# Optimization experiments

Measured on AMD Instinct MI355X. Metric: run time of the kernel, lower is better.

The kernel has to match this reference:

```python
import jax, jax.numpy as jnp
import numpy as np
from jax import lax


def setup_inputs() -> dict:
    key = jax.random.key(0)
    k1, k2 = jax.random.split(key)
    X = jax.random.normal(k1, (32, 64, 112, 112), dtype=jnp.float32)
    # module draws K ~ N(0, 0.01) each forward; we materialize it as a param
    K = 0.01 * jax.random.normal(k2, (128, 64, 3, 3), dtype=jnp.float32)
    return {"X": X, "K": K}


def reference(X, K):
    # Valid-padding cross-correlation, NCHW input, OIHW kernel, no bias.
    # Matches conv2d_multi_out: sum over in_channels, stack over out_channels.
    return lax.conv_general_dilated(
        X, K,
        window_strides=(1, 1),
        padding="VALID",
        dimension_numbers=("NCHW", "OIHW", "NCHW"),
    )
```

## Files before the change

### kernel.cpp

```cpp
#include <hip/hip_runtime.h>


typedef __attribute__((ext_vector_type(8)))  _Float16 f16x8;
typedef __attribute__((ext_vector_type(16))) float    f32x16;

typedef __attribute__((address_space(3))) uint       lds_u32;
typedef __attribute__((address_space(1))) const uint glb_u32;

constexpr int C_IN = 64, H = 112, W = 112;
constexpr int COUT = 128, OH = 110, OW = 110;
constexpr int NIMG = 32;
constexpr int KTOT = C_IN * 9;
constexpr int OSP  = OH * OW;
constexpr int SPTOT = NIMG * OSP;
constexpr int IMG_STRIDE = C_IN * H * W;
constexpr int CH_STRIDE  = H * W;
constexpr int XROW = W * C_IN;
constexpr int SLOTS = 136;
constexpr int UNITS = SLOTS * 8;
constexpr size_t A16_BYTES = (size_t)KTOT * COUT * 2;

__device__ __forceinline__ uint pkrtz_u32(float lo, float hi) {
    union { __fp16 __attribute__((ext_vector_type(2))) h; uint u; } c;
    c.h = __builtin_amdgcn_cvt_pkrtz(lo, hi);
    return c.u;
}

__global__ void prep_a(const float* __restrict__ Kw, _Float16* __restrict__ A16) {
    int idx = blockIdx.x * 256 + threadIdx.x;
    if (idx >= COUT * KTOT) return;
    int cout = idx / KTOT, k = idx - cout * KTOT;
    int c = k / 9, s = k - c * 9;
    int o = c >> 3, j = c & 7;
    A16[((size_t)(s * 8 + o) * COUT + cout) * 8 + j] = (_Float16)Kw[idx];
}

__global__ __launch_bounds__(256, 4)
void prep_x(const float* __restrict__ X, _Float16* __restrict__ X16t) {
    __shared__ _Float16 L[W * 72];
    const int t = threadIdx.x;
    const int n = blockIdx.x / H, h = blockIdx.x - n * H;
    const float* src = X + (size_t)n * IMG_STRIDE + (size_t)h * W;
    const int c = t >> 2, q = t & 3;
    const float* sc = src + (size_t)c * CH_STRIDE + q * 28;
#pragma unroll
    for (int v = 0; v < 7; v++) {
        float4 f = *reinterpret_cast<const float4*>(sc + v * 4);
        const int w0 = q * 28 + v * 4;
        L[(w0 + 0) * 72 + c] = (_Float16)f.x;
        L[(w0 + 1) * 72 + c] = (_Float16)f.y;
        L[(w0 + 2) * 72 + c] = (_Float16)f.z;
        L[(w0 + 3) * 72 + c] = (_Float16)f.w;
    }
    __syncthreads();
    _Float16* dst = X16t + ((size_t)n * H + h) * XROW;
#pragma unroll
    for (int r = 0; r < 4; r++) {
        const int u = r * 256 + t;
        if (u < 896) {
            const int w = u >> 3, sl = u & 7;
            *reinterpret_cast<f16x8*>(dst + (size_t)u * 8) =
                *reinterpret_cast<const f16x8*>(&L[w * 72 + sl * 8]);
        }
    }
}

__global__ __launch_bounds__(512, 4)
void conv_v13(const _Float16* __restrict__ X16t,
              const _Float16* __restrict__ A16,
              float* __restrict__ Out)
{
    __shared__ __align__(16) _Float16 Bs[2][SLOTS * 64];

    const int t = threadIdx.x;

    const int nwg = gridDim.x;
    const int q8 = nwg >> 3, r8 = nwg & 7;
    const int xcd = blockIdx.x & 7, idx8 = blockIdx.x >> 3;
    const int bid = (xcd < r8 ? xcd * (q8 + 1) : r8 * (q8 + 1) + (xcd - r8) * q8) + idx8;
    const int spBase = bid * 128;

    const int n0  = spBase / OSP;
    const int r0  = spBase - n0 * OSP;
    const int oh0 = r0 / OW;
    const int ow0 = r0 - oh0 * OW;
    const int seg1len = (109 - oh0) * 112 + (112 - ow0);

    const int lane = t & 63;
    const int wv   = t >> 6;
    const _Float16* sU0;
    const _Float16* sU1;
    const _Float16* sU2;
    {
        const int uu[3] = {t, t + 512, 1024 + (t & 63)};
        const _Float16* ss[3];
#pragma unroll
        for (int i = 0; i < 3; i++) {
            const int u  = uu[i];
            const int ws = u >> 3, oct = u & 7;
            const int so = (oct ^ (ws & 7)) * 8;
            size_t lin;
            if (ws < seg1len) {
                lin = (size_t)n0 * CH_STRIDE + (size_t)(oh0 * 112 + ow0 + ws);
            } else {
                const int nn = (n0 < NIMG - 1) ? n0 + 1 : n0;
                lin = (size_t)nn * CH_STRIDE + (size_t)(ws - seg1len);
            }
            ss[i] = X16t + lin * 64 + so;
        }
        sU0 = ss[0]; sU1 = ss[1]; sU2 = ss[2];
    }

    const int wq    = wv >> 1;
    const int wc    = wv & 1;
    const int frow  = lane & 31;
    const int khalf = lane >> 5;
    const size_t arow = (size_t)(wq * 32 + frow) * 8;

    int w0i, w1i;
    {
        const int ii[2] = {wc * 64 + frow, wc * 64 + 32 + frow};
        int wx[2];
#pragma unroll
        for (int i = 0; i < 2; i++) {
            const int spg = spBase + ii[i];
            const int n   = spg / OSP;
            const int r   = spg - n * OSP;
            const int oh  = r / OW;
            const int ow  = r - oh * OW;
            wx[i] = (n == n0) ? (oh - oh0) * 112 + (ow - ow0)
                              : seg1len + oh * 112 + ow;
        }
        w0i = wx[0]; w1i = wx[1];
    }

    f32x16 acc[2];
#pragma unroll
    for (int j = 0; j < 2; j++)
#pragma unroll
        for (int e = 0; e < 16; e++) acc[j][e] = 0.f;

    f16x8 aA[4], aB[4];

#define STAGE(R, B)                                                            \
    {                                                                          \
        __builtin_amdgcn_global_load_lds((const glb_u32*)(sU0 + (R) * XROW),   \
            (lds_u32*)(&Bs[B][(size_t)t * 8]), 16, 0, 0);                      \
        __builtin_amdgcn_global_load_lds((const glb_u32*)(sU1 + (R) * XROW),   \
            (lds_u32*)(&Bs[B][(size_t)(t + 512) * 8]), 16, 0, 0);              \
        if (wv == 0)                                                           \
            __builtin_amdgcn_global_load_lds((const glb_u32*)(sU2 + (R) * XROW), \
                (lds_u32*)(&Bs[B][(size_t)(1024 + lane) * 8]), 16, 0, 0);      \
    }

#define ALOAD(DST, S)                                                          \
    {                                                                          \
        _Pragma("unroll")                                                      \
        for (int kk = 0; kk < 4; kk++)                                         \
            DST[kk] = *reinterpret_cast<const f16x8*>(                         \
                &A16[(size_t)(((S) * 8 + kk * 2 + khalf) * COUT) * 8 + arow]); \
    }

#define MFMA_SH(KW, B, AREG)                                                   \
    {                                                                          \
        const int sa = w0i + (KW);                                             \
        const int sb = w1i + (KW);                                             \
        _Pragma("unroll")                                                      \
        for (int kk = 0; kk < 4; kk++) {                                       \
            const int oct = kk * 2 + khalf;                                    \
            f16x8 b0 = *reinterpret_cast<const f16x8*>(                        \
                &Bs[B][sa * 64 + ((oct ^ (sa & 7)) << 3)]);                    \
            f16x8 b1 = *reinterpret_cast<const f16x8*>(                        \
                &Bs[B][sb * 64 + ((oct ^ (sb & 7)) << 3)]);                    \
            acc[0] = __builtin_amdgcn_mfma_f32_32x32x16_f16(AREG[kk], b0, acc[0], 0, 0, 0); \
            acc[1] = __builtin_amdgcn_mfma_f32_32x32x16_f16(AREG[kk], b1, acc[1], 0, 0, 0); \
        }                                                                      \
    }

    ALOAD(aA, 0);
    STAGE(0, 0);
    __syncthreads();

    STAGE(1, 1);
    ALOAD(aB, 1); MFMA_SH(0, 0, aA);
    ALOAD(aA, 2); MFMA_SH(1, 0, aB);
    ALOAD(aB, 3); MFMA_SH(2, 0, aA);
    __syncthreads();

    STAGE(2, 0);
    ALOAD(aA, 4); MFMA_SH(0, 1, aB);
    ALOAD(aB, 5); MFMA_SH(1, 1, aA);
    ALOAD(aA, 6); MFMA_SH(2, 1, aB);
    __syncthreads();

    ALOAD(aB, 7); MFMA_SH(0, 0, aA);
    ALOAD(aA, 8); MFMA_SH(1, 0, aB);
    MFMA_SH(2, 0, aA);

#undef STAGE
#undef ALOAD
#undef MFMA_SH

#pragma unroll
    for (int j = 0; j < 2; j++) {
        const int sp2 = spBase + wc * 64 + j * 32 + frow;
        const int n2  = sp2 / OSP;
        const int r2  = sp2 - n2 * OSP;
        float* Ob = Out + (size_t)n2 * (COUT * (size_t)OSP) + r2;
        const int cbase = wq * 32 + 4 * khalf;
#pragma unroll
        for (int reg = 0; reg < 16; reg++) {
            const int crow = cbase + (reg & 3) + 8 * (reg >> 2);
            Ob[(size_t)crow * OSP] = acc[j][reg];
        }
    }
}

extern "C" void kernel_launch(void* const* d_in, const int* in_sizes, int n_in,
                              void* d_out, int out_size, void* d_ws, size_t ws_size,
                              hipStream_t stream) {
    const float* X  = (const float*)d_in[0];
    const float* Kw = (const float*)d_in[1];
    float* Out = (float*)d_out;
    _Float16* A16  = (_Float16*)d_ws;
    _Float16* X16t = (_Float16*)((char*)d_ws + A16_BYTES);

    prep_a<<<(COUT * KTOT + 255) / 256, 256, 0, stream>>>(Kw, A16);
    prep_x<<<NIMG * H, 256, 0, stream>>>(X, X16t);
    conv_v13<<<SPTOT / 128, 512, 0, stream>>>(X16t, A16, Out);
}
```

Before: 118.8 us.

## Double spatial tile to 256 per workgroup with 2x2 MFMA register tiling

Each workgroup now covers 256 output positions instead of 128. Each wave computes a 64-channel by 64-position block through a 2x2 set of 32x32 MFMA accumulators, where before it computed 32x64. This halves the number of workgroups, doubles the reuse of each A fragment and each B fragment per load, and cuts redundant halo staging. In exchange it costs more accumulator registers, doubles the LDS buffer size (which may lower occupancy), drops the A-register double buffering, and adds bounds checks for the partial last tile.

```diff
diff --git a/kernel.cpp b/kernel.cpp
--- a/kernel.cpp
+++ b/kernel.cpp
@@ -16,8 +16,9 @@
 constexpr int IMG_STRIDE = C_IN * H * W;
 constexpr int CH_STRIDE  = H * W;
 constexpr int XROW = W * C_IN;
-constexpr int SLOTS = 136;
-constexpr int UNITS = SLOTS * 8;
+constexpr int TILE = 256;
+constexpr int NWGM = (SPTOT + TILE - 1) / TILE;
+constexpr int SLOTS = 264;
 constexpr size_t A16_BYTES = (size_t)KTOT * COUT * 2;
 
 __device__ __forceinline__ uint pkrtz_u32(float lo, float hi) {
@@ -66,39 +67,35 @@
 }
 
 __global__ __launch_bounds__(512, 4)
-void conv_v13(const _Float16* __restrict__ X16t,
+void conv_v14(const _Float16* __restrict__ X16t,
               const _Float16* __restrict__ A16,
               float* __restrict__ Out)
 {
     __shared__ __align__(16) _Float16 Bs[2][SLOTS * 64];
 
     const int t = threadIdx.x;
+    const int lane = t & 63;
+    const int wv   = t >> 6;
 
     const int nwg = gridDim.x;
     const int q8 = nwg >> 3, r8 = nwg & 7;
     const int xcd = blockIdx.x & 7, idx8 = blockIdx.x >> 3;
     const int bid = (xcd < r8 ? xcd * (q8 + 1) : r8 * (q8 + 1) + (xcd - r8) * q8) + idx8;
-    const int spBase = bid * 128;
+    const int spBase = bid * TILE;
 
     const int n0  = spBase / OSP;
     const int r0  = spBase - n0 * OSP;
     const int oh0 = r0 / OW;
     const int ow0 = r0 - oh0 * OW;
-    const int seg1len = (109 - oh0) * 112 + (112 - ow0);
-
-    const int lane = t & 63;
-    const int wv   = t >> 6;
-    const _Float16* sU0;
-    const _Float16* sU1;
-    const _Float16* sU2;
+    const int seg1len = (110 - oh0) * 112 - ow0;
+
+    const _Float16 *sU0, *sU1, *sU2, *sU3, *sU4;
     {
-        const int uu[3] = {t, t + 512, 1024 + (t & 63)};
-        const _Float16* ss[3];
-#pragma unroll
-        for (int i = 0; i < 3; i++) {
-            const int u  = uu[i];
+        const _Float16* ss[5];
+#pragma unroll
+        for (int i = 0; i < 5; i++) {
+            const int u  = (i < 4) ? (t + 512 * i) : (2048 + lane);
             const int ws = u >> 3, oct = u & 7;
-            const int so = (oct ^ (ws & 7)) * 8;
             size_t lin;
             if (ws < seg1len) {
                 lin = (size_t)n0 * CH_STRIDE + (size_t)(oh0 * 112 + ow0 + ws);
@@ -106,41 +103,46 @@
                 const int nn = (n0 < NIMG - 1) ? n0 + 1 : n0;
                 lin = (size_t)nn * CH_STRIDE + (size_t)(ws - seg1len);
             }
-            ss[i] = X16t + lin * 64 + so;
-        }
-        sU0 = ss[0]; sU1 = ss[1]; sU2 = ss[2];
-    }
-
-    const int wq    = wv >> 1;
-    const int wc    = wv & 1;
+            ss[i] = X16t + lin * 64 + ((oct ^ (ws & 7)) << 3);
+        }
+        sU0 = ss[0]; sU1 = ss[1]; sU2 = ss[2]; sU3 = ss[3]; sU4 = ss[4];
+    }
+
+    const int wq2   = wv >> 2;
+    const int wsp   = wv & 3;
     const int frow  = lane & 31;
     const int khalf = lane >> 5;
-    const size_t arow = (size_t)(wq * 32 + frow) * 8;
+    const size_t arow0 = (size_t)(wq2 * 64 + frow) * 8;
+    const size_t arow1 = (size_t)(wq2 * 64 + 32 + frow) * 8;
 
     int w0i, w1i;
     {
-        const int ii[2] = {wc * 64 + frow, wc * 64 + 32 + frow};
         int wx[2];
 #pragma unroll
-        for (int i = 0; i < 2; i++) {
-            const int spg = spBase + ii[i];
-            const int n   = spg / OSP;
-            const int r   = spg - n * OSP;
-            const int oh  = r / OW;
-            const int ow  = r - oh * OW;
-            wx[i] = (n == n0) ? (oh - oh0) * 112 + (ow - ow0)
+        for (int j = 0; j < 2; j++) {
+            const int spg = spBase + wsp * 64 + j * 32 + frow;
+            int v = 0;
+            if (spg < SPTOT) {
+                const int n  = spg / OSP;
+                const int r  = spg - n * OSP;
+                const int oh = r / OW, ow = r - oh * OW;
+                v = (n == n0) ? (oh - oh0) * 112 + (ow - ow0)
                               : seg1len + oh * 112 + ow;
+            }
+            wx[j] = v;
         }
         w0i = wx[0]; w1i = wx[1];
     }
 
-    f32x16 acc[2];
-#pragma unroll
-    for (int j = 0; j < 2; j++)
-#pragma unroll
-        for (int e = 0; e < 16; e++) acc[j][e] = 0.f;
-
-    f16x8 aA[4], aB[4];
+    f32x16 acc[2][2];
+#pragma unroll
+    for (int i = 0; i < 2; i++)
+#pragma unroll
+        for (int j = 0; j < 2; j++)
+#pragma unroll
+            for (int e = 0; e < 16; e++) acc[i][j][e] = 0.f;
+
+    f16x8 a0[4], a1[4];
 
 #define STAGE(R, B)                                                            \
     {                                                                          \
@@ -148,20 +150,26 @@
             (lds_u32*)(&Bs[B][(size_t)t * 8]), 16, 0, 0);                      \
         __builtin_amdgcn_global_load_lds((const glb_u32*)(sU1 + (R) * XROW),   \
             (lds_u32*)(&Bs[B][(size_t)(t + 512) * 8]), 16, 0, 0);              \
-        if (wv == 0)                                                           \
-            __builtin_amdgcn_global_load_lds((const glb_u32*)(sU2 + (R) * XROW), \
-                (lds_u32*)(&Bs[B][(size_t)(1024 + lane) * 8]), 16, 0, 0);      \
-    }
-
-#define ALOAD(DST, S)                                                          \
+        __builtin_amdgcn_global_load_lds((const glb_u32*)(sU2 + (R) * XROW),   \
+            (lds_u32*)(&Bs[B][(size_t)(t + 1024) * 8]), 16, 0, 0);             \
+        __builtin_amdgcn_global_load_lds((const glb_u32*)(sU3 + (R) * XROW),   \
+            (lds_u32*)(&Bs[B][(size_t)(t + 1536) * 8]), 16, 0, 0);             \
+        if (t < 64)                                                            \
+            __builtin_amdgcn_global_load_lds((const glb_u32*)(sU4 + (R) * XROW), \
+                (lds_u32*)(&Bs[B][(size_t)(2048 + lane) * 8]), 16, 0, 0);      \
+    }
+
+#define ALOAD(S)                                                               \
     {                                                                          \
         _Pragma("unroll")                                                      \
-        for (int kk = 0; kk < 4; kk++)                                         \
-            DST[kk] = *reinterpret_cast<const f16x8*>(                         \
-                &A16[(size_t)(((S) * 8 + kk * 2 + khalf) * COUT) * 8 + arow]); \
-    }
-
-#define MFMA_SH(KW, B, AREG)                                                   \
+        for (int kk = 0; kk < 4; kk++) {                                       \
+            const size_t ab = (size_t)(((S) * 8 + kk * 2 + khalf) * COUT) * 8; \
+            a0[kk] = *reinterpret_cast<const f16x8*>(&A16[ab + arow0]);        \
+            a1[kk] = *reinterpret_cast<const f16x8*>(&A16[ab + arow1]);        \
+        }                                                                      \
+    }
+
+#define MFMA_SH(KW, B)                                                         \
     {                                                                          \
         const int sa = w0i + (KW);                                             \
         const int sb = w1i + (KW);                                             \
@@ -172,30 +180,31 @@
                 &Bs[B][sa * 64 + ((oct ^ (sa & 7)) << 3)]);                    \
             f16x8 b1 = *reinterpret_cast<const f16x8*>(                        \
                 &Bs[B][sb * 64 + ((oct ^ (sb & 7)) << 3)]);                    \
-            acc[0] = __builtin_amdgcn_mfma_f32_32x32x16_f16(AREG[kk], b0, acc[0], 0, 0, 0); \
-            acc[1] = __builtin_amdgcn_mfma_f32_32x32x16_f16(AREG[kk], b1, acc[1], 0, 0, 0); \
+            acc[0][0] = __builtin_amdgcn_mfma_f32_32x32x16_f16(a0[kk], b0, acc[0][0], 0, 0, 0); \
+            acc[0][1] = __builtin_amdgcn_mfma_f32_32x32x16_f16(a0[kk], b1, acc[0][1], 0, 0, 0); \
+            acc[1][0] = __builtin_amdgcn_mfma_f32_32x32x16_f16(a1[kk], b0, acc[1][0], 0, 0, 0); \
+            acc[1][1] = __builtin_amdgcn_mfma_f32_32x32x16_f16(a1[kk], b1, acc[1][1], 0, 0, 0); \
         }                                                                      \
     }
 
-    ALOAD(aA, 0);
     STAGE(0, 0);
     __syncthreads();
 
     STAGE(1, 1);
-    ALOAD(aB, 1); MFMA_SH(0, 0, aA);
-    ALOAD(aA, 2); MFMA_SH(1, 0, aB);
-    ALOAD(aB, 3); MFMA_SH(2, 0, aA);
+    ALOAD(0); MFMA_SH(0, 0);
+    ALOAD(1); MFMA_SH(1, 0);
+    ALOAD(2); MFMA_SH(2, 0);
     __syncthreads();
 
     STAGE(2, 0);
-    ALOAD(aA, 4); MFMA_SH(0, 1, aB);
-    ALOAD(aB, 5); MFMA_SH(1, 1, aA);
-    ALOAD(aA, 6); MFMA_SH(2, 1, aB);
-    __syncthreads();
-
-    ALOAD(aB, 7); MFMA_SH(0, 0, aA);
-    ALOAD(aA, 8); MFMA_SH(1, 0, aB);
-    MFMA_SH(2, 0, aA);
+    ALOAD(3); MFMA_SH(0, 1);
+    ALOAD(4); MFMA_SH(1, 1);
+    ALOAD(5); MFMA_SH(2, 1);
+    __syncthreads();
+
+    ALOAD(6); MFMA_SH(0, 0);
+    ALOAD(7); MFMA_SH(1, 0);
+    ALOAD(8); MFMA_SH(2, 0);
 
 #undef STAGE
 #undef ALOAD
@@ -203,15 +212,20 @@
 
 #pragma unroll
     for (int j = 0; j < 2; j++) {
-        const int sp2 = spBase + wc * 64 + j * 32 + frow;
-        const int n2  = sp2 / OSP;
-        const int r2  = sp2 - n2 * OSP;
-        float* Ob = Out + (size_t)n2 * (COUT * (size_t)OSP) + r2;
-        const int cbase = wq * 32 + 4 * khalf;
-#pragma unroll
-        for (int reg = 0; reg < 16; reg++) {
-            const int crow = cbase + (reg & 3) + 8 * (reg >> 2);
-            Ob[(size_t)crow * OSP] = acc[j][reg];
+        const int sp2 = spBase + wsp * 64 + j * 32 + frow;
+        if (sp2 < SPTOT) {
+            const int n2 = sp2 / OSP;
+            const int r2 = sp2 - n2 * OSP;
+            float* Ob = Out + (size_t)n2 * (COUT * (size_t)OSP) + r2;
+#pragma unroll
+            for (int i = 0; i < 2; i++) {
+                const int cbase = wq2 * 64 + i * 32 + 4 * khalf;
+#pragma unroll
+                for (int reg = 0; reg < 16; reg++) {
+                    const int crow = cbase + (reg & 3) + 8 * (reg >> 2);
+                    Ob[(size_t)crow * OSP] = acc[i][j][reg];
+                }
+            }
         }
     }
 }
@@ -227,5 +241,5 @@
 
     prep_a<<<(COUT * KTOT + 255) / 256, 256, 0, stream>>>(Kw, A16);
     prep_x<<<NIMG * H, 256, 0, stream>>>(X, X16t);
-    conv_v13<<<SPTOT / 128, 512, 0, stream>>>(X16t, A16, Out);
-}
+    conv_v14<<<NWGM, 512, 0, stream>>>(X16t, A16, Out);
+}
```

New measurement: 137.4 us. 1.16x slower.
